# Performance work log

Hardware: AMD Instinct MI355X
Metric: run time of the kernel (lower is better)

Reference implementation:

```python
import jax, jax.numpy as jnp
import numpy as np

N_HEADS = 16


def setup_inputs() -> dict:
    key = jax.random.key(0)
    k1, k2, k3 = jax.random.split(key, 3)
    b, t, d = 2, 2048, 1024
    x = jax.random.normal(k1, (b, t, d), dtype=jnp.float32)
    # nn.Linear weights (stored here as [in, out]); 0.02 scale ~ standard init
    w_qkv = jax.random.normal(k2, (d, 3 * d), dtype=jnp.float32) * 0.02
    w_out = jax.random.normal(k3, (d, d), dtype=jnp.float32) * 0.02
    return {"x": x, "w_qkv": w_qkv, "w_out": w_out}


def reference(x, w_qkv, w_out):
    # Causal multi-head self-attention. The original module implements this
    # via a hand-rolled blockwise flash-attention loop with online softmax;
    # the intended math is exactly standard causal SDPA, expressed densely here.
    b, t, d = x.shape
    h = N_HEADS
    hd = d // h
    qkv = (x @ w_qkv).reshape(b, t, 3, h, hd)
    qkv = jnp.transpose(qkv, (2, 0, 3, 1, 4))  # [3, b, h, t, hd]
    q, k, v = qkv[0], qkv[1], qkv[2]
    scale = 1.0 / jnp.sqrt(jnp.float32(hd))
    s = jnp.einsum("bhqd,bhkd->bhqk", q, k) * scale  # [b, h, t, t]
    causal = jnp.tril(jnp.ones((t, t), dtype=bool))
    s = jnp.where(causal, s, -jnp.inf)
    p = jax.nn.softmax(s, axis=-1)
    o = jnp.einsum("bhqk,bhkd->bhqd", p, v)
    o = jnp.transpose(o, (0, 2, 1, 3)).reshape(b, t, d)
    return o @ w_out
```

## Files before the change

kernel.cpp:

```cpp
#include <hip/hip_runtime.h>

typedef float f32x4 __attribute__((ext_vector_type(4)));
typedef float f32x16 __attribute__((ext_vector_type(16)));
typedef short short8 __attribute__((ext_vector_type(8)));
typedef short short4_t __attribute__((ext_vector_type(4)));

#define GLOAD_LDS16(gp, lp) \
  __builtin_amdgcn_global_load_lds((const __attribute__((address_space(1))) void*)(gp), \
                                   (__attribute__((address_space(3))) void*)(lp), 16, 0, 0)

__device__ __forceinline__ short f2bf(float f){
  unsigned u = __builtin_bit_cast(unsigned, f);
  u += 0x7fffu + ((u >> 16) & 1u);
  return (short)(u >> 16);
}

__device__ __forceinline__ float exp2_fast(float x){
  return __builtin_amdgcn_exp2f(x);
}

__global__ __launch_bounds__(256) void prep_kernel(
    const float* __restrict__ x, const float* __restrict__ wqkv,
    const float* __restrict__ wout, short* __restrict__ xb,
    short* __restrict__ wqkvT, short* __restrict__ woutT)
{
  __shared__ float tile[32][33];
  const int bid = blockIdx.x, tid = threadIdx.x;
  if (bid < 512){
    int base = bid*2048 + tid;
    #pragma unroll
    for (int it=0; it<8; it++){
      int i = base + it*256;
      f32x4 v = ((const f32x4*)x)[i];
      short4_t s;
      s[0]=f2bf(v[0]); s[1]=f2bf(v[1]); s[2]=f2bf(v[2]); s[3]=f2bf(v[3]);
      ((short4_t*)xb)[i] = s;
    }
    return;
  }
  const float* w; short* wT; int N, idx;
  if (bid < 3584){ w = wqkv; wT = wqkvT; N = 3072; idx = bid - 512;  }
  else           { w = wout; wT = woutT; N = 1024; idx = bid - 3584; }
  const int K = 1024;
  int bn = (idx % (N >> 5)) * 32, bk = (idx / (N >> 5)) * 32;
  int tx = tid & 31, ty = tid >> 5;
  #pragma unroll
  for (int r=ty; r<32; r+=8) tile[r][tx] = w[(size_t)(bk+r)*N + bn + tx];
  __syncthreads();
  #pragma unroll
  for (int r=ty; r<32; r+=8) wT[(size_t)(bn+r)*K + bk + tx] = f2bf(tile[tx][r]);
}

template<int MODE>
__global__ __launch_bounds__(256) void gemm128_kernel(
    const short* __restrict__ A, const short* __restrict__ Bt,
    float* __restrict__ Cf, short* __restrict__ qb_, short* __restrict__ kb_,
    short* __restrict__ vtb, int M, int N, int K)
{
  __shared__ short a_lds[128*64];
  __shared__ short b_lds[128*64];
  const int tid = threadIdx.x;
  const int lane = tid & 63;
  const int l15 = lane & 15, lg = lane >> 4;
  const int w  = tid >> 6;
  const int wr = w >> 1, wc = w & 1;
  const int m0 = blockIdx.x * 128, n0 = blockIdx.y * 128;

  f32x4 acc[4][4];
  #pragma unroll
  for (int i=0;i<4;i++)
    #pragma unroll
    for (int j=0;j<4;j++) acc[i][j] = (f32x4){0.f,0.f,0.f,0.f};

  for (int kt = 0; kt < K; kt += 64){
    __syncthreads();
    #pragma unroll
    for (int i=0;i<4;i++){
      int u = i*256 + tid;
      int row = u >> 3, cu = u & 7;
      int kl = ((cu ^ (row & 7)) << 3);
      GLOAD_LDS16(A + (size_t)(m0+row)*K + kt + kl, a_lds + (size_t)(i*256 + (tid & ~63))*8);
    }
    #pragma unroll
    for (int i=0;i<4;i++){
      int u = i*256 + tid;
      int row = u >> 3, cu = u & 7;
      int kl = ((cu ^ (row & 7)) << 3);
      GLOAD_LDS16(Bt + (size_t)(n0+row)*K + kt + kl, b_lds + (size_t)(i*256 + (tid & ~63))*8);
    }
    asm volatile("s_waitcnt vmcnt(0)" ::: "memory");
    __syncthreads();

    #pragma unroll
    for (int kk=0;kk<2;kk++){
      short8 af[4], bfr[4];
      #pragma unroll
      for (int mi=0;mi<4;mi++){
        int row = wr*64 + mi*16 + l15;
        int uu = ((kk*4 + lg) ^ (row & 7));
        af[mi] = *(const short8*)&a_lds[row*64 + uu*8];
      }
      #pragma unroll
      for (int ni=0;ni<4;ni++){
        int row = wc*64 + ni*16 + l15;
        int uu = ((kk*4 + lg) ^ (row & 7));
        bfr[ni] = *(const short8*)&b_lds[row*64 + uu*8];
      }
      #pragma unroll
      for (int mi=0;mi<4;mi++)
        #pragma unroll
        for (int ni=0;ni<4;ni++)
          acc[mi][ni] = __builtin_amdgcn_mfma_f32_16x16x32_bf16(af[mi], bfr[ni], acc[mi][ni], 0,0,0);
    }
  }

  #pragma unroll
  for (int mi=0;mi<4;mi++){
    #pragma unroll
    for (int ni=0;ni<4;ni++){
      int col = n0 + wc*64 + ni*16 + l15;
      #pragma unroll
      for (int r=0;r<4;r++){
        int rowg = m0 + wr*64 + mi*16 + lg*4 + r;
        float v = acc[mi][ni][r];
        if (MODE == 0){
          Cf[(size_t)rowg*N + col] = v;
        } else {
          int three = col >> 10, hh = (col >> 6) & 15, e = col & 63;
          int bb = rowg >> 11, t = rowg & 2047;
          int bh = bb*16 + hh;
          if (three == 0)      qb_[((size_t)bh*2048 + t)*64 + e] = f2bf(v * (0.125f*1.44269504f));
          else if (three == 1) kb_[((size_t)bh*2048 + t)*64 + e] = f2bf(v);
          else                 vtb[((size_t)bh*64 + e)*2048 + t] = f2bf(v);
        }
      }
    }
  }
}

__global__ __launch_bounds__(256) void attn_kernel(
    const short* __restrict__ q, const short* __restrict__ kbuf,
    const short* __restrict__ vt, short* __restrict__ ob)
{
  __shared__ short k_lds[2][128*64];
  __shared__ short v_lds[2][64*128];

  const int tid = threadIdx.x, lane = tid & 63, w = tid >> 6;
  const int l31 = lane & 31, hi = lane >> 5;
  const int qi = blockIdx.x >> 5;
  const int qb = (qi < 8) ? (15 - qi) : (qi - 8);
  const int bh = blockIdx.x & 31;
  const int q0 = qb * 128;

  const short* qg = q + ((size_t)bh*2048 + q0 + w*32 + l31)*64 + hi*8;
  short8 qf[4];
  #pragma unroll
  for (int kk=0;kk<4;kk++) qf[kk] = *(const short8*)(qg + kk*16);

  f32x16 o_acc[2];
  #pragma unroll
  for (int oc=0;oc<2;oc++)
    #pragma unroll
    for (int r=0;r<16;r++) o_acc[oc][r] = 0.f;
  float mreg = -1e30f, lreg = 0.f;

  const int sw = l31 & 7;
  int kro[4], vro[8];
  #pragma unroll
  for (int kk=0;kk<4;kk++) kro[kk] = l31*128 + (((kk*2+hi)^sw) << 4);
  #pragma unroll
  for (int ks=0;ks<8;ks++) vro[ks] = l31*256 + (((ks*2+hi)^sw) << 4);

  const int xk = ((tid & 7) ^ ((tid >> 3) & 7)) * 8;
  const int xv = ((tid & 15) ^ ((tid >> 4) & 7)) * 8;
  const short* kp = kbuf + (size_t)bh*2048*64 + (size_t)(tid >> 3)*64 + xk;
  const short* vp = vt   + (size_t)bh*64*2048 + (size_t)(tid >> 4)*2048 + xv;
  const int dst = (tid & ~63)*8;

  const int n = qb + 1;
  #pragma unroll
  for (int i=0;i<4;i++) GLOAD_LDS16(kp + i*2048,  &k_lds[0][i*2048 + dst]);
  #pragma unroll
  for (int i=0;i<4;i++) GLOAD_LDS16(vp + i*32768, &v_lds[0][i*2048 + dst]);
  kp += 8192; vp += 128;

  for (int s = 0; s < n; s++){
    const int cur = s & 1;
    if (s + 1 < n){
      #pragma unroll
      for (int i=0;i<4;i++) GLOAD_LDS16(kp + i*2048,  &k_lds[cur^1][i*2048 + dst]);
      #pragma unroll
      for (int i=0;i<4;i++) GLOAD_LDS16(vp + i*32768, &v_lds[cur^1][i*2048 + dst]);
      kp += 8192; vp += 128;
      asm volatile("s_waitcnt vmcnt(8)" ::: "memory");
    } else {
      asm volatile("s_waitcnt vmcnt(0)" ::: "memory");
    }
    __builtin_amdgcn_s_barrier();

    const char* kl_ = (const char*)&k_lds[cur][0];
    const char* vl_ = (const char*)&v_lds[cur][0];

    f32x16 sacc[4];
    #pragma unroll
    for (int ct=0;ct<4;ct++)
      #pragma unroll
      for (int r=0;r<16;r++) sacc[ct][r] = 0.f;
    __builtin_amdgcn_s_setprio(1);
    #pragma unroll
    for (int kk=0;kk<4;kk++){
      #pragma unroll
      for (int ct=0;ct<4;ct++){
        short8 kf = *(const short8*)(kl_ + kro[kk] + ct*4096);
        sacc[ct] = __builtin_amdgcn_mfma_f32_32x32x16_bf16(kf, qf[kk], sacc[ct], 0,0,0);
      }
    }
    __builtin_amdgcn_s_setprio(0);

    if (s == qb){
      const int qloc = w*32 + l31 - 4*hi;
      #pragma unroll
      for (int ct=0;ct<4;ct++)
        #pragma unroll
        for (int r=0;r<16;r++)
          if (ct*32 + (r&3) + 8*(r>>2) > qloc) sacc[ct][r] = -1e30f;
    }

    float pmax = sacc[0][0];
    #pragma unroll
    for (int ct=0;ct<4;ct++)
      #pragma unroll
      for (int r=0;r<16;r++) pmax = fmaxf(pmax, sacc[ct][r]);
    pmax = fmaxf(pmax, __shfl_xor(pmax, 32));

    if (!__all(pmax - mreg <= 8.0f)){
      float mnew = fmaxf(mreg, pmax);
      float alpha = exp2_fast(mreg - mnew);
      mreg = mnew;
      lreg *= alpha;
      float aRow[16];
      #pragma unroll
      for (int r=0;r<16;r++) aRow[r] = __shfl(alpha, (r&3) + 8*(r>>2) + 4*hi);
      #pragma unroll
      for (int oc=0;oc<2;oc++)
        #pragma unroll
        for (int r=0;r<16;r++) o_acc[oc][r] *= aRow[r];
    }

    float sum = 0.f;
    #pragma unroll
    for (int ct=0;ct<4;ct++){
      float pv[16];
      #pragma unroll
      for (int r=0;r<16;r++){ pv[r] = exp2_fast(sacc[ct][r] - mreg); sum += pv[r]; }
      unsigned pk[8];
      #pragma unroll
      for (int t=0;t<8;t++)
        asm("v_cvt_pk_bf16_f32 %0, %1, %2" : "=v"(pk[t]) : "v"(pv[2*t]), "v"(pv[2*t+1]));
      #pragma unroll
      for (int kss=0;kss<2;kss++){
        const int W = 4*kss;
        unsigned x0 = pk[W],   x2 = pk[W+2];
        unsigned x1 = pk[W+1], x3 = pk[W+3];
        asm("v_permlane32_swap_b32 %0, %1" : "+v"(x0), "+v"(x2));
        asm("v_permlane32_swap_b32 %0, %1" : "+v"(x1), "+v"(x3));
        uint4 pau = {x0, x1, x2, x3};
        short8 pa = __builtin_bit_cast(short8, pau);
        __builtin_amdgcn_s_setprio(1);
        #pragma unroll
        for (int oc=0;oc<2;oc++){
          short8 vf = *(const short8*)(vl_ + vro[2*ct+kss] + oc*8192);
          o_acc[oc] = __builtin_amdgcn_mfma_f32_32x32x16_bf16(pa, vf, o_acc[oc], 0,0,0);
        }
        __builtin_amdgcn_s_setprio(0);
      }
    }
    sum += __shfl_xor(sum, 32);
    lreg += sum;

    __builtin_amdgcn_s_barrier();
  }

  const int bb = bh >> 4, hh = bh & 15;
  #pragma unroll
  for (int r=0;r<16;r++){
    float lf = __shfl(lreg, (r&3) + 8*(r>>2) + 4*hi);
    float inv = 1.0f / lf;
    int t = q0 + w*32 + (r&3) + 8*(r>>2) + 4*hi;
    size_t base = ((size_t)(bb*2048 + t))*1024 + (size_t)hh*64 + l31;
    ob[base]      = f2bf(o_acc[0][r] * inv);
    ob[base + 32] = f2bf(o_acc[1][r] * inv);
  }
}

extern "C" void kernel_launch(void* const* d_in, const int* in_sizes, int n_in,
                              void* d_out, int out_size, void* d_ws, size_t ws_size,
                              hipStream_t stream) {
  const float* x     = (const float*)d_in[0];
  const float* w_qkv = (const float*)d_in[1];
  const float* w_out = (const float*)d_in[2];
  float* out = (float*)d_out;

  char* ws = (char*)d_ws;
  short* xb    = (short*)(ws);
  short* wqkvT = (short*)(ws + (8u  << 20));
  short* woutT = (short*)(ws + (14u << 20));
  short* qbuf  = (short*)(ws + (16u << 20));
  short* kbuf  = (short*)(ws + (24u << 20));
  short* vtbuf = (short*)(ws + (32u << 20));
  short* obuf  = (short*)(ws + (40u << 20));

  prep_kernel<<<4608, 256, 0, stream>>>(x, w_qkv, w_out, xb, wqkvT, woutT);
  gemm128_kernel<1><<<dim3(32,24), 256, 0, stream>>>(xb, wqkvT, nullptr,
                                                     qbuf, kbuf, vtbuf, 4096, 3072, 1024);
  attn_kernel<<<dim3(512), 256, 0, stream>>>(qbuf, kbuf, vtbuf, obuf);
  gemm128_kernel<0><<<dim3(32,8), 256, 0, stream>>>(obuf, woutT, out,
                                                    nullptr, nullptr, nullptr, 4096, 1024, 1024);
}
```

Baseline: 112.9 us.

## Split attention KV tile across two wave groups and merge softmax partials

The attention block grows from 4 to 8 waves. Each pair of waves shares the same 32 query rows, and each wave processes half of the 128 keys in every KV tile. This halves the per-wave QK and PV work per tile and doubles the waves resident per block, to hide latency better. At the end, the second group writes its partial max, sum and output to LDS, and the first group merges them with a rescaled online-softmax combine. The cost is an extra LDS exchange and a synchronisation, plus redundant Q loads and softmax bookkeeping.

```diff
diff --git a/kernel.cpp b/kernel.cpp
--- a/kernel.cpp
+++ b/kernel.cpp
@@ -138,21 +138,23 @@
   }
 }
 
-__global__ __launch_bounds__(256) void attn_kernel(
+__global__ __launch_bounds__(512) void attn_kernel(
     const short* __restrict__ q, const short* __restrict__ kbuf,
     const short* __restrict__ vt, short* __restrict__ ob)
 {
-  __shared__ short k_lds[2][128*64];
-  __shared__ short v_lds[2][64*128];
+  __shared__ short sm[2*128*64 + 2*64*128];
+  short* k_lds = sm;
+  short* v_lds = sm + 2*128*64;
 
   const int tid = threadIdx.x, lane = tid & 63, w = tid >> 6;
+  const int wg = w & 3, g = w >> 2;
   const int l31 = lane & 31, hi = lane >> 5;
   const int qi = blockIdx.x >> 5;
   const int qb = (qi < 8) ? (15 - qi) : (qi - 8);
   const int bh = blockIdx.x & 31;
   const int q0 = qb * 128;
 
-  const short* qg = q + ((size_t)bh*2048 + q0 + w*32 + l31)*64 + hi*8;
+  const short* qg = q + ((size_t)bh*2048 + q0 + wg*32 + l31)*64 + hi*8;
   short8 qf[4];
   #pragma unroll
   for (int kk=0;kk<4;kk++) qf[kk] = *(const short8*)(qg + kk*16);
@@ -165,11 +167,11 @@
   float mreg = -1e30f, lreg = 0.f;
 
   const int sw = l31 & 7;
-  int kro[4], vro[8];
-  #pragma unroll
-  for (int kk=0;kk<4;kk++) kro[kk] = l31*128 + (((kk*2+hi)^sw) << 4);
-  #pragma unroll
-  for (int ks=0;ks<8;ks++) vro[ks] = l31*256 + (((ks*2+hi)^sw) << 4);
+  int kro[4], vro[4];
+  #pragma unroll
+  for (int kk=0;kk<4;kk++) kro[kk] = g*8192 + l31*128 + (((kk*2+hi)^sw) << 4);
+  #pragma unroll
+  for (int ks=0;ks<4;ks++) vro[ks] = g*128  + l31*256 + (((ks*2+hi)^sw) << 4);
 
   const int xk = ((tid & 7) ^ ((tid >> 3) & 7)) * 8;
   const int xv = ((tid & 15) ^ ((tid >> 4) & 7)) * 8;
@@ -179,56 +181,56 @@
 
   const int n = qb + 1;
   #pragma unroll
-  for (int i=0;i<4;i++) GLOAD_LDS16(kp + i*2048,  &k_lds[0][i*2048 + dst]);
-  #pragma unroll
-  for (int i=0;i<4;i++) GLOAD_LDS16(vp + i*32768, &v_lds[0][i*2048 + dst]);
+  for (int i=0;i<2;i++) GLOAD_LDS16(kp + i*4096,  k_lds + i*4096 + dst);
+  #pragma unroll
+  for (int i=0;i<2;i++) GLOAD_LDS16(vp + i*65536, v_lds + i*4096 + dst);
   kp += 8192; vp += 128;
 
   for (int s = 0; s < n; s++){
     const int cur = s & 1;
     if (s + 1 < n){
       #pragma unroll
-      for (int i=0;i<4;i++) GLOAD_LDS16(kp + i*2048,  &k_lds[cur^1][i*2048 + dst]);
-      #pragma unroll
-      for (int i=0;i<4;i++) GLOAD_LDS16(vp + i*32768, &v_lds[cur^1][i*2048 + dst]);
+      for (int i=0;i<2;i++) GLOAD_LDS16(kp + i*4096,  k_lds + (cur^1)*8192 + i*4096 + dst);
+      #pragma unroll
+      for (int i=0;i<2;i++) GLOAD_LDS16(vp + i*65536, v_lds + (cur^1)*8192 + i*4096 + dst);
       kp += 8192; vp += 128;
-      asm volatile("s_waitcnt vmcnt(8)" ::: "memory");
+      asm volatile("s_waitcnt vmcnt(4)" ::: "memory");
     } else {
       asm volatile("s_waitcnt vmcnt(0)" ::: "memory");
     }
     __builtin_amdgcn_s_barrier();
 
-    const char* kl_ = (const char*)&k_lds[cur][0];
-    const char* vl_ = (const char*)&v_lds[cur][0];
-
-    f32x16 sacc[4];
-    #pragma unroll
-    for (int ct=0;ct<4;ct++)
+    const char* klp = (const char*)(k_lds + cur*8192);
+    const char* vlp = (const char*)(v_lds + cur*8192);
+
+    f32x16 sacc[2];
+    #pragma unroll
+    for (int ct=0;ct<2;ct++)
       #pragma unroll
       for (int r=0;r<16;r++) sacc[ct][r] = 0.f;
     __builtin_amdgcn_s_setprio(1);
     #pragma unroll
     for (int kk=0;kk<4;kk++){
       #pragma unroll
-      for (int ct=0;ct<4;ct++){
-        short8 kf = *(const short8*)(kl_ + kro[kk] + ct*4096);
+      for (int ct=0;ct<2;ct++){
+        short8 kf = *(const short8*)(klp + kro[kk] + ct*4096);
         sacc[ct] = __builtin_amdgcn_mfma_f32_32x32x16_bf16(kf, qf[kk], sacc[ct], 0,0,0);
       }
     }
     __builtin_amdgcn_s_setprio(0);
 
     if (s == qb){
-      const int qloc = w*32 + l31 - 4*hi;
-      #pragma unroll
-      for (int ct=0;ct<4;ct++)
+      const int qloc = wg*32 + l31 - 4*hi;
+      #pragma unroll
+      for (int ct=0;ct<2;ct++)
         #pragma unroll
         for (int r=0;r<16;r++)
-          if (ct*32 + (r&3) + 8*(r>>2) > qloc) sacc[ct][r] = -1e30f;
+          if (g*64 + ct*32 + (r&3) + 8*(r>>2) > qloc) sacc[ct][r] = -1e30f;
     }
 
     float pmax = sacc[0][0];
     #pragma unroll
-    for (int ct=0;ct<4;ct++)
+    for (int ct=0;ct<2;ct++)
       #pragma unroll
       for (int r=0;r<16;r++) pmax = fmaxf(pmax, sacc[ct][r]);
     pmax = fmaxf(pmax, __shfl_xor(pmax, 32));
@@ -249,7 +251,7 @@
 
     float sum = 0.f;
     #pragma unroll
-    for (int ct=0;ct<4;ct++){
+    for (int ct=0;ct<2;ct++){
       float pv[16];
       #pragma unroll
       for (int r=0;r<16;r++){ pv[r] = exp2_fast(sacc[ct][r] - mreg); sum += pv[r]; }
@@ -269,7 +271,7 @@
         __builtin_amdgcn_s_setprio(1);
         #pragma unroll
         for (int oc=0;oc<2;oc++){
-          short8 vf = *(const short8*)(vl_ + vro[2*ct+kss] + oc*8192);
+          short8 vf = *(const short8*)(vlp + vro[2*ct+kss] + oc*8192);
           o_acc[oc] = __builtin_amdgcn_mfma_f32_32x32x16_bf16(pa, vf, o_acc[oc], 0,0,0);
         }
         __builtin_amdgcn_s_setprio(0);
@@ -281,15 +283,45 @@
     __builtin_amdgcn_s_barrier();
   }
 
-  const int bb = bh >> 4, hh = bh & 15;
-  #pragma unroll
-  for (int r=0;r<16;r++){
-    float lf = __shfl(lreg, (r&3) + 8*(r>>2) + 4*hi);
-    float inv = 1.0f / lf;
-    int t = q0 + w*32 + (r&3) + 8*(r>>2) + 4*hi;
-    size_t base = ((size_t)(bb*2048 + t))*1024 + (size_t)hh*64 + l31;
-    ob[base]      = f2bf(o_acc[0][r] * inv);
-    ob[base + 32] = f2bf(o_acc[1][r] * inv);
+  float* cmb = (float*)sm;
+  if (g == 1){
+    float* bse = cmb + wg*2176;
+    bse[lane] = mreg;
+    bse[64 + lane] = lreg;
+    #pragma unroll
+    for (int oc=0;oc<2;oc++)
+      #pragma unroll
+      for (int r=0;r<16;r++) bse[(2 + oc*16 + r)*64 + lane] = o_acc[oc][r];
+  }
+  __syncthreads();
+  if (g == 0){
+    float* bse = cmb + wg*2176;
+    float m1 = bse[lane], l1 = bse[64 + lane];
+    float mN = fmaxf(mreg, m1);
+    float s0 = exp2_fast(mreg - mN), s1 = exp2_fast(m1 - mN);
+    float lt = s0*lreg + s1*l1;
+    float s0R[16], s1R[16];
+    #pragma unroll
+    for (int r=0;r<16;r++){
+      int src = (r&3) + 8*(r>>2) + 4*hi;
+      s0R[r] = __shfl(s0, src); s1R[r] = __shfl(s1, src);
+    }
+    #pragma unroll
+    for (int oc=0;oc<2;oc++)
+      #pragma unroll
+      for (int r=0;r<16;r++)
+        o_acc[oc][r] = s0R[r]*o_acc[oc][r] + s1R[r]*bse[(2 + oc*16 + r)*64 + lane];
+
+    const int bb = bh >> 4, hh = bh & 15;
+    #pragma unroll
+    for (int r=0;r<16;r++){
+      float lf = __shfl(lt, (r&3) + 8*(r>>2) + 4*hi);
+      float inv = 1.0f / lf;
+      int t = q0 + wg*32 + (r&3) + 8*(r>>2) + 4*hi;
+      size_t base = ((size_t)(bb*2048 + t))*1024 + (size_t)hh*64 + l31;
+      ob[base]      = f2bf(o_acc[0][r] * inv);
+      ob[base + 32] = f2bf(o_acc[1][r] * inv);
+    }
   }
 }
 
@@ -313,7 +345,7 @@
   prep_kernel<<<4608, 256, 0, stream>>>(x, w_qkv, w_out, xb, wqkvT, woutT);
   gemm128_kernel<1><<<dim3(32,24), 256, 0, stream>>>(xb, wqkvT, nullptr,
                                                      qbuf, kbuf, vtbuf, 4096, 3072, 1024);
-  attn_kernel<<<dim3(512), 256, 0, stream>>>(qbuf, kbuf, vtbuf, obuf);
+  attn_kernel<<<dim3(512), 512, 0, stream>>>(qbuf, kbuf, vtbuf, obuf);
   gemm128_kernel<0><<<dim3(32,8), 256, 0, stream>>>(obuf, woutT, out,
                                                     nullptr, nullptr, nullptr, 4096, 1024, 1024);
 }
```

New measurement: 103.7 us (median of 2 runs). -8.1%, faster.
